# Optimization experiments

Hardware: AMD Instinct MI355X
Metric: run time of the kernel (lower is better)

Reference implementation:

```python
import jax, jax.numpy as jnp
import numpy as np

N = 50000            # nodes (cells)
E_RAND = 1_600_000   # random edges; self loops appended -> E = E_RAND + N
DIMS = [(512, 384), (384, 256), (256, 128)]  # (in, hidden) per encoder stage
OUT = 128


def setup_inputs() -> dict:
    key = jax.random.key(0)
    ks = jax.random.split(key, 16)
    features = jax.random.normal(ks[0], (N, DIMS[0][0]), dtype=jnp.float32)
    src = jax.random.randint(ks[1], (E_RAND,), 0, N, dtype=jnp.int32)
    dst = jax.random.randint(ks[2], (E_RAND,), 0, N, dtype=jnp.int32)
    loops = jnp.arange(N, dtype=jnp.int32)  # dgl.add_self_loop
    src = jnp.concatenate([src, loops])
    dst = jnp.concatenate([dst, loops])
    inp = {"features": features, "src": src, "dst": dst}
    i = 3
    for s, (din, dout) in enumerate(DIMS):
        inp[f"sage_w{s}"] = jax.random.normal(ks[i], (dout, din), jnp.float32) / np.sqrt(din); i += 1
        inp[f"sage_b{s}"] = jnp.zeros((dout,), jnp.float32)
        inp[f"gc_w{s}"] = jax.random.normal(ks[i], (dout, dout), jnp.float32) / np.sqrt(dout); i += 1
        inp[f"gc_b{s}"] = jnp.zeros((dout,), jnp.float32)
    inp["fc_w"] = jax.random.normal(ks[i], (OUT, DIMS[-1][1]), jnp.float32) / np.sqrt(DIMS[-1][1])
    inp["fc_b"] = jnp.zeros((OUT,), jnp.float32)
    return inp


def reference(features, src, dst,
              sage_w0, sage_b0, gc_w0, gc_b0,
              sage_w1, sage_b1, gc_w1, gc_b1,
              sage_w2, sage_b2, gc_w2, gc_b2,
              fc_w, fc_b):
    ones = jnp.ones((src.shape[0],), jnp.float32)
    in_deg = jax.ops.segment_sum(ones, dst, num_segments=N)
    out_deg = jax.ops.segment_sum(ones, src, num_segments=N)
    # GraphConv norm='both' scalers (clamp degree to >=1, as DGL does)
    inv_src = jnp.where(out_deg > 0, out_deg, 1.0) ** -0.5  # [N]
    inv_dst = jnp.where(in_deg > 0, in_deg, 1.0) ** -0.5    # [N]
    sage_den = (in_deg + 1.0)[:, None]                      # SAGE 'gcn' denominator

    def sage_gcn(h, w, b):
        # DGL SAGEConv aggregator_type='gcn': (sum_neigh + self)/(in_deg+1) -> fc_neigh
        agg = jax.ops.segment_sum(h[src], dst, num_segments=N)
        return ((agg + h) / sage_den) @ w.T + b

    def graph_conv(h, w, b):
        # DGL GraphConv norm='both': D_out^{-1/2} -> sum aggregate -> D_in^{-1/2} -> W
        hn = h * inv_src[:, None]
        agg = jax.ops.segment_sum(hn[src], dst, num_segments=N)
        return (agg * inv_dst[:, None]) @ w.T + b

    params = [(sage_w0, sage_b0, gc_w0, gc_b0),
              (sage_w1, sage_b1, gc_w1, gc_b1),
              (sage_w2, sage_b2, gc_w2, gc_b2)]
    h = features
    for sw, sb, gw, gb in params:
        h = jax.nn.relu(sage_gcn(h, sw, sb))
        h = jax.nn.relu(graph_conv(h, gw, gb))
    return h @ fc_w.T + fc_b
```

## Files before the change

kernel.cpp:

```cpp
#include <hip/hip_runtime.h>
#include <cstddef>
#include <cstdint>


typedef _Float16 h8 __attribute__((ext_vector_type(8)));
typedef _Float16 h4 __attribute__((ext_vector_type(4)));
typedef float f32x4 __attribute__((ext_vector_type(4)));

#define HB 64


__global__ __launch_bounds__(256) void deg_kernel(
    const int* __restrict__ dst, int* __restrict__ in_deg,
    int* __restrict__ ord, int E) {
  int e = blockIdx.x * 256 + threadIdx.x;
  if (e < E) ord[e] = atomicAdd(&in_deg[dst[e]], 1);
}

__global__ __launch_bounds__(1024) void histo_out_kernel(
    const int* __restrict__ src, uint32_t* __restrict__ H, int E, int bins2) {
  __shared__ uint32_t hh[25088];
  for (int i = threadIdx.x; i < bins2; i += 1024) hh[i] = 0;
  __syncthreads();
  const int C = (E + HB - 1) / HB;
  const int base = blockIdx.x * C;
  int lim = base + C; if (lim > E) lim = E;
  for (int e = base + (int)threadIdx.x; e < lim; e += 1024) {
    int s = src[e];
    atomicAdd(&hh[s >> 1], 1u << ((s & 1) * 16));
  }
  __syncthreads();
  uint32_t* out = H + (size_t)blockIdx.x * bins2;
  for (int i = threadIdx.x; i < bins2; i += 1024) out[i] = hh[i];
}

__global__ __launch_bounds__(256) void reduce_out_kernel(
    const uint32_t* __restrict__ H, int* __restrict__ out_deg,
    int bins2, int n) {
  int i = blockIdx.x * 256 + threadIdx.x;
  if (i >= bins2) return;
  uint32_t lo = 0, hi = 0;
  for (int b = 0; b < HB; ++b) {
    uint32_t v = H[(size_t)b * bins2 + i];
    lo += v & 0xFFFFu;
    hi += v >> 16;
  }
  out_deg[2 * i] = (int)lo;
  if (2 * i + 1 < n) out_deg[2 * i + 1] = (int)hi;
}


__global__ __launch_bounds__(256) void scan_a(
    const int* __restrict__ deg, int* __restrict__ bsum, int n) {
  __shared__ int s[256];
  int i = blockIdx.x * 256 + threadIdx.x;
  s[threadIdx.x] = (i < n) ? deg[i] : 0;
  __syncthreads();
  #pragma unroll
  for (int off = 128; off > 0; off >>= 1) {
    if ((int)threadIdx.x < off) s[threadIdx.x] += s[threadIdx.x + off];
    __syncthreads();
  }
  if (threadIdx.x == 0) bsum[blockIdx.x] = s[0];
}

__global__ __launch_bounds__(256) void scan_b(
    int* __restrict__ bsum, int* __restrict__ rp, int nb, int n) {
  __shared__ int s[256];
  const int t = threadIdx.x;
  int v = (t < nb) ? bsum[t] : 0;
  s[t] = v;
  __syncthreads();
  #pragma unroll
  for (int off = 1; off < 256; off <<= 1) {
    int a = (t >= off) ? s[t - off] : 0;
    __syncthreads();
    s[t] += a;
    __syncthreads();
  }
  bsum[256 + t] = s[t] - v;
  if (t == 255) rp[n] = s[255];
}

__global__ __launch_bounds__(256) void scan_c(
    const int* __restrict__ in_deg, const int* __restrict__ out_deg,
    const int* __restrict__ bsum, int* __restrict__ rp,
    float* __restrict__ inv_src, float* __restrict__ inv_dst,
    float* __restrict__ inv_den, int n) {
  __shared__ int s[256];
  const int t = threadIdx.x;
  const int i = blockIdx.x * 256 + t;
  int v = (i < n) ? in_deg[i] : 0;
  s[t] = v;
  __syncthreads();
  #pragma unroll
  for (int off = 1; off < 256; off <<= 1) {
    int a = (t >= off) ? s[t - off] : 0;
    __syncthreads();
    s[t] += a;
    __syncthreads();
  }
  if (i < n) {
    rp[i] = bsum[256 + blockIdx.x] + s[t] - v;
    float od = (float)out_deg[i];
    float id = (float)v;
    inv_src[i] = rsqrtf(od > 0.f ? od : 1.0f);
    inv_dst[i] = rsqrtf(id > 0.f ? id : 1.0f);
    inv_den[i] = 1.0f / (id + 1.0f);
  }
}

__global__ __launch_bounds__(256) void scatter_kernel(
    const int* __restrict__ src, const int* __restrict__ dst,
    const int* __restrict__ rp, const int* __restrict__ ord,
    int* __restrict__ csr, int E) {
  int e = blockIdx.x * 256 + threadIdx.x;
  if (e < E) csr[rp[dst[e]] + ord[e]] = src[e];
}


__global__ __launch_bounds__(256) void cvt_kernel(
    const float* __restrict__ in, _Float16* __restrict__ out,
    long n_in, long n_pad) {
  long i = ((long)blockIdx.x * 256 + (long)threadIdx.x) * 4;
  if (i >= n_pad) return;
  float4 v = (i < n_in) ? *(const float4*)(in + i) : make_float4(0.f, 0.f, 0.f, 0.f);
  h4 h = {(_Float16)v.x, (_Float16)v.y, (_Float16)v.z, (_Float16)v.w};
  *(h4*)(out + i) = h;
}

struct WArgs {
  const float* s[7];
  _Float16* d[7];
  int n[7];
};

__global__ __launch_bounds__(256) void wcvt_kernel(WArgs a) {
  const int w = blockIdx.y;
  long i = ((long)blockIdx.x * 256 + (long)threadIdx.x) * 4;
  if (i >= a.n[w]) return;
  float4 v = *(const float4*)(a.s[w] + i);
  h4 h = {(_Float16)v.x, (_Float16)v.y, (_Float16)v.z, (_Float16)v.w};
  *(h4*)(a.d[w] + i) = h;
}


__device__ __forceinline__ void gload_lds16(const _Float16* g, _Float16* l) {
  __builtin_amdgcn_global_load_lds(
      (const __attribute__((address_space(1))) void*)g,
      (__attribute__((address_space(3))) void*)l, 16, 0, 0);
}


template <typename OutT>
__global__ __launch_bounds__(256) void hgemm(
    const _Float16* __restrict__ A, const _Float16* __restrict__ W,
    OutT* __restrict__ C, int Mstore, int K, int Nc,
    const float* __restrict__ row_scale, const float* __restrict__ bias) {
  __shared__ _Float16 As[128 * 32];
  __shared__ _Float16 Bs[128 * 32];
  const int tid = threadIdx.x;
  const int bm = blockIdx.x * 128, bn = blockIdx.y * 128;
  const int wave = tid >> 6, lane = tid & 63;
  const int wm = (wave & 1) * 64, wn = (wave >> 1) * 64;
  const int lrow = lane & 15, lq = lane >> 4;

  const int r0 = tid >> 2;
  const int cc = (tid & 3) * 8;
  const _Float16* Ag = A + (size_t)(bm + r0) * K + cc;
  const _Float16* Wg = W + (size_t)(bn + r0) * K + cc;
  const size_t rs64 = (size_t)64 * K;
  _Float16* As0 = As + tid * 8;
  _Float16* As1 = As + 64 * 32 + tid * 8;
  _Float16* Bs0 = Bs + tid * 8;
  _Float16* Bs1 = Bs + 64 * 32 + tid * 8;

  f32x4 acc[4][4];
  #pragma unroll
  for (int i = 0; i < 4; ++i)
    #pragma unroll
    for (int j = 0; j < 4; ++j) acc[i][j] = (f32x4){0.f, 0.f, 0.f, 0.f};

  for (int k0 = 0; k0 < K; k0 += 32) {
    __syncthreads();
    gload_lds16(Ag + k0, As0);
    gload_lds16(Ag + rs64 + k0, As1);
    gload_lds16(Wg + k0, Bs0);
    gload_lds16(Wg + rs64 + k0, Bs1);
    __syncthreads();
    h8 af[4], bf[4];
    #pragma unroll
    for (int i = 0; i < 4; ++i)
      af[i] = *(const h8*)(As + (wm + i * 16 + lrow) * 32 + lq * 8);
    #pragma unroll
    for (int j = 0; j < 4; ++j)
      bf[j] = *(const h8*)(Bs + (wn + j * 16 + lrow) * 32 + lq * 8);
    #pragma unroll
    for (int i = 0; i < 4; ++i)
      #pragma unroll
      for (int j = 0; j < 4; ++j)
        acc[i][j] = __builtin_amdgcn_mfma_f32_16x16x32_f16(af[i], bf[j], acc[i][j], 0, 0, 0);
  }

  #pragma unroll
  for (int i = 0; i < 4; ++i) {
    #pragma unroll
    for (int r = 0; r < 4; ++r) {
      const int m = bm + wm + i * 16 + lq * 4 + r;
      if (m < Mstore) {
        const float rsc = row_scale ? row_scale[m] : 1.0f;
        OutT* crow = C + (size_t)m * Nc + bn + wn + lrow;
        #pragma unroll
        for (int j = 0; j < 4; ++j) {
          float v = acc[i][j][r] * rsc;
          if (bias) v += bias[bn + wn + j * 16 + lrow];
          crow[j * 16] = (OutT)v;
        }
      }
    }
  }
}


template <int D, bool SELF>
__global__ __launch_bounds__(256) void agg_h(
    const _Float16* __restrict__ Z, const int* __restrict__ row_ptr,
    const int* __restrict__ csr, const float* __restrict__ out_scale,
    const float* __restrict__ bias, _Float16* __restrict__ out, int n) {
  constexpr int CH = D / 8;
  constexpr int GROUP = 16;
  constexpr int NV = CH / GROUP;
  const int gid = threadIdx.x >> 4;
  const int lane = threadIdx.x & 15;
  const int node = blockIdx.x * 16 + gid;
  if (node >= n) return;

  const int rs = row_ptr[node], re = row_ptr[node + 1];

  float acc[NV][8];
  #pragma unroll
  for (int v = 0; v < NV; ++v)
    #pragma unroll
    for (int q = 0; q < 8; ++q) acc[v][q] = 0.f;

  for (int e = rs; e < re; e += GROUP) {
    int m = re - e; if (m > GROUP) m = GROUP;
    int eid = (lane < m) ? csr[e + lane] : 0;
    for (int j = 0; j < m; ++j) {
      int s = __shfl(eid, j, GROUP);
      const h8* zr = (const h8*)(Z + (size_t)s * D);
      #pragma unroll
      for (int v = 0; v < NV; ++v) {
        h8 t = zr[lane + v * GROUP];
        #pragma unroll
        for (int q = 0; q < 8; ++q) acc[v][q] += (float)t[q];
      }
    }
  }

  const float osc = out_scale[node];
  const h8* zs = (const h8*)(Z + (size_t)node * D);
  _Float16* orow = out + (size_t)node * D;
  #pragma unroll
  for (int v = 0; v < NV; ++v) {
    const int idx = lane + v * GROUP;
    if (SELF) {
      h8 t = zs[idx];
      #pragma unroll
      for (int q = 0; q < 8; ++q) acc[v][q] += (float)t[q];
    }
    h8 r;
    #pragma unroll
    for (int q = 0; q < 8; ++q) {
      float x = acc[v][q] * osc + bias[idx * 8 + q];
      r[q] = (_Float16)fmaxf(x, 0.f);
    }
    *(h8*)(orow + idx * 8) = r;
  }
}


extern "C" void kernel_launch(void* const* d_in, const int* in_sizes, int n_in,
                              void* d_out, int out_size, void* d_ws, size_t ws_size,
                              hipStream_t stream) {
  const float* features = (const float*)d_in[0];
  const int*   src      = (const int*)d_in[1];
  const int*   dst      = (const int*)d_in[2];
  const float* wsrc[7] = {(const float*)d_in[3],  (const float*)d_in[5],
                          (const float*)d_in[7],  (const float*)d_in[9],
                          (const float*)d_in[11], (const float*)d_in[13],
                          (const float*)d_in[15]};
  const float* sb[3] = {(const float*)d_in[4],  (const float*)d_in[8],  (const float*)d_in[12]};
  const float* gb[3] = {(const float*)d_in[6],  (const float*)d_in[10], (const float*)d_in[14]};
  const float* fc_b  = (const float*)d_in[16];

  const int N = in_sizes[0] / 512;
  const int E = in_sizes[1];
  const int MB = (N + 127) / 128;
  const int Mpad = MB * 128;
  const int bins2 = (N + 1) / 2;
  if (bins2 > 25088) return;

  const int wcnt[7] = {384 * 512, 384 * 384, 256 * 384, 256 * 256,
                       128 * 256, 128 * 128, 128 * 128};

  char* ws = (char*)d_ws;
  _Float16* featH = (_Float16*)ws;
  _Float16* hA    = featH + (size_t)Mpad * 512;
  _Float16* hB    = hA + (size_t)Mpad * 384;
  _Float16* wH[7];
  {
    _Float16* p = hB + (size_t)Mpad * 384;
    for (int i = 0; i < 7; ++i) { wH[i] = p; p += wcnt[i]; }
  }
  int* csr     = (int*)(wH[6] + wcnt[6]);
  int* rp      = csr + E;
  int* in_dg   = rp + (N + 1);
  int* out_dg  = in_dg + N;
  int* sblk    = out_dg + N;
  float* inv_src = (float*)(sblk + N);
  float* inv_dst = inv_src + N;
  float* inv_den = inv_dst + N;

  int*      ord = (int*)hB;
  uint32_t* H64 = (uint32_t*)(ord + E);

  size_t totw = 0; for (int i = 0; i < 7; ++i) totw += wcnt[i];
  size_t needed = ((size_t)Mpad * (512 + 384 + 384) + totw) * 2 +
                  ((size_t)E + (N + 1) + 6 * (size_t)N) * 4;
  if (ws_size < needed) return;

  (void)hipMemsetAsync(in_dg, 0, sizeof(int) * (size_t)N, stream);

  const int eb = (E + 255) / 256;
  const int nb256 = (N + 255) / 256;

  deg_kernel<<<eb, 256, 0, stream>>>(dst, in_dg, ord, E);
  histo_out_kernel<<<HB, 1024, 0, stream>>>(src, H64, E, bins2);
  reduce_out_kernel<<<(bins2 + 255) / 256, 256, 0, stream>>>(H64, out_dg, bins2, N);
  scan_a<<<nb256, 256, 0, stream>>>(in_dg, sblk, N);
  scan_b<<<1, 256, 0, stream>>>(sblk, rp, nb256, N);
  scan_c<<<nb256, 256, 0, stream>>>(in_dg, out_dg, sblk, rp,
                                    inv_src, inv_dst, inv_den, N);
  scatter_kernel<<<eb, 256, 0, stream>>>(src, dst, rp, ord, csr, E);

  {
    long thr = (long)Mpad * 512 / 4;
    cvt_kernel<<<(int)((thr + 255) / 256), 256, 0, stream>>>(
        features, featH, (long)N * 512, (long)Mpad * 512);
    WArgs wa;
    int maxn = 0;
    for (int i = 0; i < 7; ++i) {
      wa.s[i] = wsrc[i]; wa.d[i] = wH[i]; wa.n[i] = wcnt[i];
      if (wcnt[i] > maxn) maxn = wcnt[i];
    }
    dim3 wg((maxn / 4 + 255) / 256, 7);
    wcvt_kernel<<<wg, 256, 0, stream>>>(wa);
  }

  const int dout[3] = {384, 256, 128};
  const _Float16* h = featH;
  int K = 512;
  for (int s = 0; s < 3; ++s) {
    const int D = dout[s];
    dim3 gg(MB, D / 128);
    const int ab = (N + 15) / 16;
    hgemm<_Float16><<<gg, 256, 0, stream>>>(h, wH[2 * s], hB, Mpad, K, D, nullptr, nullptr);
    if (D == 384)      agg_h<384, true><<<ab, 256, 0, stream>>>(hB, rp, csr, inv_den, sb[s], hA, N);
    else if (D == 256) agg_h<256, true><<<ab, 256, 0, stream>>>(hB, rp, csr, inv_den, sb[s], hA, N);
    else               agg_h<128, true><<<ab, 256, 0, stream>>>(hB, rp, csr, inv_den, sb[s], hA, N);
    hgemm<_Float16><<<gg, 256, 0, stream>>>(hA, wH[2 * s + 1], hB, Mpad, D, D, inv_src, nullptr);
    if (D == 384)      agg_h<384, false><<<ab, 256, 0, stream>>>(hB, rp, csr, inv_dst, gb[s], hA, N);
    else if (D == 256) agg_h<256, false><<<ab, 256, 0, stream>>>(hB, rp, csr, inv_dst, gb[s], hA, N);
    else               agg_h<128, false><<<ab, 256, 0, stream>>>(hB, rp, csr, inv_dst, gb[s], hA, N);
    h = hA;
    K = D;
  }
  dim3 gf(MB, 1);
  hgemm<float><<<gf, 256, 0, stream>>>(h, wH[6], (float*)d_out, N, 128, 128, nullptr, fc_b);
}
```

Measured before the change: 1.192 ms.

## Build CSR via per-chunk LDS histograms instead of global atomics; grid-stride aggregation

Replaces the global-atomic in-degree/ordering pass with 256 chunked LDS histograms that record per-chunk ranks. A column scan over chunks produces per-chunk offsets and in-degrees, and the scatter adds those offsets back in. This removes contended global atomics on 50k counters, at the cost of extra histogram memory traffic and 16-bit packed counters that could overflow on skewed degrees. The aggregation kernel also becomes grid-stride with half as many blocks, so each 16-lane group handles two nodes.

```diff
diff --git a/kernel.cpp b/kernel.cpp
--- a/kernel.cpp
+++ b/kernel.cpp
@@ -8,13 +8,26 @@
 typedef float f32x4 __attribute__((ext_vector_type(4)));
 
 #define HB 64
-
-
-__global__ __launch_bounds__(256) void deg_kernel(
-    const int* __restrict__ dst, int* __restrict__ in_deg,
-    int* __restrict__ ord, int E) {
-  int e = blockIdx.x * 256 + threadIdx.x;
-  if (e < E) ord[e] = atomicAdd(&in_deg[dst[e]], 1);
+#define NCH 256
+
+
+__global__ __launch_bounds__(1024) void histo_dst_kernel(
+    const int* __restrict__ dst, uint32_t* __restrict__ H,
+    int* __restrict__ ord, int E, int bins2, int CE) {
+  __shared__ uint32_t hh[25088];
+  for (int i = threadIdx.x; i < bins2; i += 1024) hh[i] = 0;
+  __syncthreads();
+  const int base = blockIdx.x * CE;
+  int lim = base + CE; if (lim > E) lim = E;
+  for (int e = base + (int)threadIdx.x; e < lim; e += 1024) {
+    int d = dst[e];
+    const int sh = (d & 1) * 16;
+    uint32_t old = atomicAdd(&hh[d >> 1], 1u << sh);
+    ord[e] = (int)((old >> sh) & 0xFFFFu);
+  }
+  __syncthreads();
+  uint32_t* out = H + (size_t)blockIdx.x * bins2;
+  for (int i = threadIdx.x; i < bins2; i += 1024) out[i] = hh[i];
 }
 
 __global__ __launch_bounds__(1024) void histo_out_kernel(
@@ -49,6 +62,22 @@
   if (2 * i + 1 < n) out_deg[2 * i + 1] = (int)hi;
 }
 
+__global__ __launch_bounds__(256) void chunk_scan_kernel(
+    uint32_t* __restrict__ H, int* __restrict__ in_deg, int bins2, int n) {
+  int i = blockIdx.x * 256 + threadIdx.x;
+  if (i >= bins2) return;
+  uint32_t lo = 0, hi = 0;
+  for (int c = 0; c < NCH; ++c) {
+    uint32_t* p = H + (size_t)c * bins2 + i;
+    uint32_t v = *p;
+    *p = lo | (hi << 16);
+    lo += v & 0xFFFFu;
+    hi += v >> 16;
+  }
+  in_deg[2 * i] = (int)lo;
+  if (2 * i + 1 < n) in_deg[2 * i + 1] = (int)hi;
+}
+
 
 __global__ __launch_bounds__(256) void scan_a(
     const int* __restrict__ deg, int* __restrict__ bsum, int n) {
@@ -110,12 +139,22 @@
   }
 }
 
-__global__ __launch_bounds__(256) void scatter_kernel(
+__global__ __launch_bounds__(1024) void scatter_kernel(
     const int* __restrict__ src, const int* __restrict__ dst,
     const int* __restrict__ rp, const int* __restrict__ ord,
-    int* __restrict__ csr, int E) {
-  int e = blockIdx.x * 256 + threadIdx.x;
-  if (e < E) csr[rp[dst[e]] + ord[e]] = src[e];
+    const uint32_t* __restrict__ H, int* __restrict__ csr,
+    int E, int bins2, int CE) {
+  __shared__ uint32_t hh[25088];
+  const uint32_t* Hc = H + (size_t)blockIdx.x * bins2;
+  for (int i = threadIdx.x; i < bins2; i += 1024) hh[i] = Hc[i];
+  __syncthreads();
+  const int base = blockIdx.x * CE;
+  int lim = base + CE; if (lim > E) lim = E;
+  for (int e = base + (int)threadIdx.x; e < lim; e += 1024) {
+    int d = dst[e];
+    int b = (int)((hh[d >> 1] >> ((d & 1) * 16)) & 0xFFFFu);
+    csr[rp[d] + b + ord[e]] = src[e];
+  }
 }
 
 
@@ -232,50 +271,51 @@
   constexpr int NV = CH / GROUP;
   const int gid = threadIdx.x >> 4;
   const int lane = threadIdx.x & 15;
-  const int node = blockIdx.x * 16 + gid;
-  if (node >= n) return;
-
-  const int rs = row_ptr[node], re = row_ptr[node + 1];
-
-  float acc[NV][8];
-  #pragma unroll
-  for (int v = 0; v < NV; ++v)
-    #pragma unroll
-    for (int q = 0; q < 8; ++q) acc[v][q] = 0.f;
-
-  for (int e = rs; e < re; e += GROUP) {
-    int m = re - e; if (m > GROUP) m = GROUP;
-    int eid = (lane < m) ? csr[e + lane] : 0;
-    for (int j = 0; j < m; ++j) {
-      int s = __shfl(eid, j, GROUP);
-      const h8* zr = (const h8*)(Z + (size_t)s * D);
+  const int stride = gridDim.x * 16;
+
+  for (int node = blockIdx.x * 16 + gid; node < n; node += stride) {
+    const int rs = row_ptr[node], re = row_ptr[node + 1];
+
+    float acc[NV][8];
+    #pragma unroll
+    for (int v = 0; v < NV; ++v)
       #pragma unroll
-      for (int v = 0; v < NV; ++v) {
-        h8 t = zr[lane + v * GROUP];
+      for (int q = 0; q < 8; ++q) acc[v][q] = 0.f;
+
+    for (int e = rs; e < re; e += GROUP) {
+      int m = re - e; if (m > GROUP) m = GROUP;
+      int eid = (lane < m) ? csr[e + lane] : 0;
+      for (int j = 0; j < m; ++j) {
+        int s = __shfl(eid, j, GROUP);
+        const h8* zr = (const h8*)(Z + (size_t)s * D);
+        #pragma unroll
+        for (int v = 0; v < NV; ++v) {
+          h8 t = zr[lane + v * GROUP];
+          #pragma unroll
+          for (int q = 0; q < 8; ++q) acc[v][q] += (float)t[q];
+        }
+      }
+    }
+
+    const float osc = out_scale[node];
+    const h8* zs = (const h8*)(Z + (size_t)node * D);
+    _Float16* orow = out + (size_t)node * D;
+    #pragma unroll
+    for (int v = 0; v < NV; ++v) {
+      const int idx = lane + v * GROUP;
+      if (SELF) {
+        h8 t = zs[idx];
         #pragma unroll
         for (int q = 0; q < 8; ++q) acc[v][q] += (float)t[q];
       }
+      h8 r;
+      #pragma unroll
+      for (int q = 0; q < 8; ++q) {
+        float x = acc[v][q] * osc + bias[idx * 8 + q];
+        r[q] = (_Float16)fmaxf(x, 0.f);
+      }
+      *(h8*)(orow + idx * 8) = r;
     }
-  }
-
-  const float osc = out_scale[node];
-  const h8* zs = (const h8*)(Z + (size_t)node * D);
-  _Float16* orow = out + (size_t)node * D;
-  #pragma unroll
-  for (int v = 0; v < NV; ++v) {
-    const int idx = lane + v * GROUP;
-    if (SELF) {
-      h8 t = zs[idx];
-      #pragma unroll
-      for (int q = 0; q < 8; ++q) acc[v][q] += (float)t[q];
-    }
-    h8 r;
-    #pragma unroll
-    for (int q = 0; q < 8; ++q) {
-      float x = acc[v][q] * osc + bias[idx * 8 + q];
-      r[q] = (_Float16)fmaxf(x, 0.f);
-    }
-    *(h8*)(orow + idx * 8) = r;
   }
 }
 
@@ -322,27 +362,29 @@
   float* inv_dst = inv_src + N;
   float* inv_den = inv_dst + N;
 
-  int*      ord = (int*)hB;
-  uint32_t* H64 = (uint32_t*)(ord + E);
+  int*      ord  = (int*)hB;
+  uint32_t* Hsrc = (uint32_t*)(ord + E);
+  uint32_t* Hdst = (uint32_t*)hA;
 
   size_t totw = 0; for (int i = 0; i < 7; ++i) totw += wcnt[i];
   size_t needed = ((size_t)Mpad * (512 + 384 + 384) + totw) * 2 +
                   ((size_t)E + (N + 1) + 6 * (size_t)N) * 4;
   if (ws_size < needed) return;
 
-  (void)hipMemsetAsync(in_dg, 0, sizeof(int) * (size_t)N, stream);
-
-  const int eb = (E + 255) / 256;
+  const int CE = (E + NCH - 1) / NCH;
   const int nb256 = (N + 255) / 256;
-
-  deg_kernel<<<eb, 256, 0, stream>>>(dst, in_dg, ord, E);
-  histo_out_kernel<<<HB, 1024, 0, stream>>>(src, H64, E, bins2);
-  reduce_out_kernel<<<(bins2 + 255) / 256, 256, 0, stream>>>(H64, out_dg, bins2, N);
+  const int binsb = (bins2 + 255) / 256;
+
+  histo_dst_kernel<<<NCH, 1024, 0, stream>>>(dst, Hdst, ord, E, bins2, CE);
+  histo_out_kernel<<<HB, 1024, 0, stream>>>(src, Hsrc, E, bins2);
+  chunk_scan_kernel<<<binsb, 256, 0, stream>>>(Hdst, in_dg, bins2, N);
+  reduce_out_kernel<<<binsb, 256, 0, stream>>>(Hsrc, out_dg, bins2, N);
   scan_a<<<nb256, 256, 0, stream>>>(in_dg, sblk, N);
   scan_b<<<1, 256, 0, stream>>>(sblk, rp, nb256, N);
   scan_c<<<nb256, 256, 0, stream>>>(in_dg, out_dg, sblk, rp,
                                     inv_src, inv_dst, inv_den, N);
-  scatter_kernel<<<eb, 256, 0, stream>>>(src, dst, rp, ord, csr, E);
+  scatter_kernel<<<NCH, 1024, 0, stream>>>(src, dst, rp, ord, Hdst, csr,
+                                           E, bins2, CE);
 
   {
     long thr = (long)Mpad * 512 / 4;
@@ -361,10 +403,10 @@
   const int dout[3] = {384, 256, 128};
   const _Float16* h = featH;
   int K = 512;
+  const int ab = (N + 31) / 32;
   for (int s = 0; s < 3; ++s) {
     const int D = dout[s];
     dim3 gg(MB, D / 128);
-    const int ab = (N + 15) / 16;
     hgemm<_Float16><<<gg, 256, 0, stream>>>(h, wH[2 * s], hB, Mpad, K, D, nullptr, nullptr);
     if (D == 384)      agg_h<384, true><<<ab, 256, 0, stream>>>(hB, rp, csr, inv_den, sb[s], hA, N);
     else if (D == 256) agg_h<256, true><<<ab, 256, 0, stream>>>(hB, rp, csr, inv_den, sb[s], hA, N);
```

After: 1.178 ms. About the same (-1.2%).
